# Kernel tuning notes

Measured on AMD Instinct MI355X. Metric: run time of the kernel, lower is better.

The kernel has to match this reference:

```python
import jax, jax.numpy as jnp
import numpy as np

B, D, H, E, K = 4096, 1024, 4096, 8, 2

def setup_inputs() -> dict:
    key = jax.random.key(0)
    ks = jax.random.split(key, 6)
    return {
        "x_modality": jax.random.normal(ks[0], (B, D), dtype=jnp.float32),
        "expert_indices": jax.random.randint(ks[1], (B, K), 0, E, dtype=jnp.int32),
        "hard_weights": jax.random.uniform(ks[2], (B, K), dtype=jnp.float32),
        "w1": jax.random.normal(ks[3], (E, D, H), dtype=jnp.float32) * (1.0 / np.sqrt(D)),
        "b1": jnp.zeros((E, H), dtype=jnp.float32),
        "w2": jax.random.normal(ks[4], (E, H, D), dtype=jnp.float32) * (1.0 / np.sqrt(H)),
        "b2": jnp.zeros((E, D), dtype=jnp.float32),
    }

def reference(x_modality, expert_indices, hard_weights, w1, b1, w2, b2):
    b = x_modality.shape[0]
    # Per-token gate per expert: sum of hard_weights over top_k slots routed to that expert.
    gates = jnp.zeros((b, E), dtype=x_modality.dtype)
    gates = gates.at[jnp.arange(b)[:, None], expert_indices].add(hard_weights)  # [b, E]
    # Dense expert compute (small fixed E), then gated combine.
    h = jax.nn.gelu(jnp.einsum("bd,edh->ebh", x_modality, w1) + b1[:, None, :], approximate=False)
    y = jnp.einsum("ebh,ehd->ebd", h, w2) + b2[:, None, :]  # [E, b, D]
    return jnp.einsum("be,ebd->bd", gates, y)
```

## Files before the change

kernel.cpp:

```cpp
#include <hip/hip_runtime.h>
#include <hip/hip_bf16.h>
#include <math.h>

#define NB 4096
#define ND 1024
#define NH 4096
#define NE 8
#define NKK 2
#define NROWS (NB*NKK)

typedef __attribute__((ext_vector_type(8))) short short8;
typedef __attribute__((ext_vector_type(4))) float f32x4;

__device__ __forceinline__ void gload_lds16(const void* g, void* l) {
    __builtin_amdgcn_global_load_lds(
        (const __attribute__((address_space(1))) unsigned int*)g,
        (__attribute__((address_space(3))) unsigned int*)l, 16, 0, 0);
}

__device__ __forceinline__ unsigned short f2bf(float f) {
    __hip_bfloat16 h = __float2bfloat16(f);
    return *reinterpret_cast<unsigned short*>(&h);
}


__global__ void k_cvt_x(const float* __restrict__ in, __hip_bfloat16* __restrict__ out, int n8) {
    int i = blockIdx.x * 256 + threadIdx.x;
    if (i >= n8) return;
    const float4* p = reinterpret_cast<const float4*>(in) + (size_t)i * 2;
    float4 a = p[0], b = p[1];
    ushort4 lo, hi;
    lo.x = f2bf(a.x); lo.y = f2bf(a.y); lo.z = f2bf(a.z); lo.w = f2bf(a.w);
    hi.x = f2bf(b.x); hi.y = f2bf(b.y); hi.z = f2bf(b.z); hi.w = f2bf(b.w);
    reinterpret_cast<ushort4*>(out)[(size_t)i*2]   = lo;
    reinterpret_cast<ushort4*>(out)[(size_t)i*2+1] = hi;
}

__global__ void k_transpose_cvt(const float* __restrict__ in, __hip_bfloat16* __restrict__ out,
                                int R, int C) {
    __shared__ float tile[64][65];
    const size_t ebase = (size_t)blockIdx.z * R * C;
    const int r0 = blockIdx.y * 64, c0 = blockIdx.x * 64;
    const int tx = threadIdx.x & 63, tg = threadIdx.x >> 6;
    #pragma unroll
    for (int i = 0; i < 16; ++i) {
        int r = tg + i * 4;
        tile[r][tx] = in[ebase + (size_t)(r0 + r) * C + (c0 + tx)];
    }
    __syncthreads();
    const int q = threadIdx.x & 15, cw = threadIdx.x >> 4;
    #pragma unroll
    for (int i = 0; i < 4; ++i) {
        int c = cw + i * 16;
        ushort4 v;
        v.x = f2bf(tile[q*4+0][c]);
        v.y = f2bf(tile[q*4+1][c]);
        v.z = f2bf(tile[q*4+2][c]);
        v.w = f2bf(tile[q*4+3][c]);
        *reinterpret_cast<ushort4*>(&out[ebase + (size_t)(c0 + c) * R + (r0 + q*4)]) = v;
    }
}


__global__ void k_route_count(const int* __restrict__ idx, int* cnt) {
    int b = blockIdx.x * 256 + threadIdx.x;
    if (b < NB) {
        atomicAdd(&cnt[idx[2*b]], 1);
        atomicAdd(&cnt[idx[2*b+1]], 1);
    }
}

__global__ void k_route_scan(const int* __restrict__ cnt, int* offs, int* cursor) {
    if (threadIdx.x == 0) {
        int s = 0;
        for (int e = 0; e < NE; ++e) { offs[e] = s; cursor[e] = s; s += cnt[e]; }
        offs[NE] = s;
    }
}

__global__ void k_route_fill(const int* __restrict__ idx, const float* __restrict__ hw,
                             int* cursor, int* tok, float* gw) {
    int b = blockIdx.x * 256 + threadIdx.x;
    if (b < NB) {
        #pragma unroll
        for (int k = 0; k < NKK; ++k) {
            int e = idx[2*b + k];
            int p = atomicAdd(&cursor[e], 1);
            tok[p] = b;
            gw[p]  = hw[2*b + k];
        }
    }
}


template<int STAGE>
__global__ __launch_bounds__(256, 2) void moe_gemm(
    const __hip_bfloat16* __restrict__ Asrc,
    const __hip_bfloat16* __restrict__ Bt,
    const float* __restrict__ bias,
    __hip_bfloat16* __restrict__ Hout,
    float* __restrict__ Out,
    const int* __restrict__ offs,
    const int* __restrict__ tok,
    const float* __restrict__ gw)
{
    constexpr int N = (STAGE == 1) ? NH : ND;
    constexpr int K = (STAGE == 1) ? ND : NH;

    const int e = blockIdx.z;
    const int end = offs[e + 1];
    const int rowbase = offs[e] + blockIdx.y * 128;
    if (rowbase >= end) return;
    const int nt = blockIdx.x;

    __shared__ __align__(16) __hip_bfloat16 sA[128 * 64];
    __shared__ __align__(16) __hip_bfloat16 sB[128 * 64];

    const int tid = threadIdx.x;
    const int w = tid >> 6;
    const int l = tid & 63;

    const int srow = tid >> 3;
    const int schunk = (tid & 7) ^ (srow & 7);
    const __hip_bfloat16* aptr[4];
    const __hip_bfloat16* bptr[4];
    #pragma unroll
    for (int i = 0; i < 4; ++i) {
        int r = srow + i * 32;
        int re = rowbase + r; if (re > end - 1) re = end - 1;
        if (STAGE == 1) aptr[i] = Asrc + (size_t)tok[re] * ND + schunk * 8;
        else            aptr[i] = Asrc + (size_t)re * NH + schunk * 8;
        bptr[i] = Bt + ((size_t)e * N + (nt * 128 + r)) * K + schunk * 8;
    }
    __hip_bfloat16 *adst[4], *bdst[4];
    #pragma unroll
    for (int i = 0; i < 4; ++i) {
        adst[i] = sA + (i * 256 + w * 64) * 8;
        bdst[i] = sB + (i * 256 + w * 64) * 8;
    }

    const int wm = (w >> 1) * 64;
    const int wn = (w & 1) * 64;
    const int l15 = l & 15, l4 = l >> 4;

    f32x4 acc[4][4];
    #pragma unroll
    for (int mi = 0; mi < 4; ++mi)
        #pragma unroll
        for (int ni = 0; ni < 4; ++ni) acc[mi][ni] = (f32x4){0.f, 0.f, 0.f, 0.f};

    int aoff[4][2], boff[4][2];
    #pragma unroll
    for (int mi = 0; mi < 4; ++mi) {
        int row = wm + mi * 16 + l15;
        #pragma unroll
        for (int ks = 0; ks < 2; ++ks)
            aoff[mi][ks] = row * 128 + (((ks * 4 + l4) ^ (row & 7)) * 16);
    }
    #pragma unroll
    for (int ni = 0; ni < 4; ++ni) {
        int row = wn + ni * 16 + l15;
        #pragma unroll
        for (int ks = 0; ks < 2; ++ks)
            boff[ni][ks] = row * 128 + (((ks * 4 + l4) ^ (row & 7)) * 16);
    }

    const char* sAb = (const char*)sA;
    const char* sBb = (const char*)sB;

    for (int kt = 0; kt < K / 64; ++kt) {
        #pragma unroll
        for (int i = 0; i < 4; ++i) {
            gload_lds16(aptr[i] + kt * 64, adst[i]);
            gload_lds16(bptr[i] + kt * 64, bdst[i]);
        }
        __syncthreads();
        short8 af[4][2], bfr[4][2];
        #pragma unroll
        for (int mi = 0; mi < 4; ++mi)
            #pragma unroll
            for (int ks = 0; ks < 2; ++ks)
                af[mi][ks] = *(const short8*)(sAb + aoff[mi][ks]);
        #pragma unroll
        for (int ni = 0; ni < 4; ++ni)
            #pragma unroll
            for (int ks = 0; ks < 2; ++ks)
                bfr[ni][ks] = *(const short8*)(sBb + boff[ni][ks]);
        #pragma unroll
        for (int mi = 0; mi < 4; ++mi)
            #pragma unroll
            for (int ni = 0; ni < 4; ++ni)
                #pragma unroll
                for (int ks = 0; ks < 2; ++ks)
                    acc[mi][ni] = __builtin_amdgcn_mfma_f32_16x16x32_bf16(
                        af[mi][ks], bfr[ni][ks], acc[mi][ni], 0, 0, 0);
        __syncthreads();
    }

    const int ncol0 = nt * 128 + wn;
    #pragma unroll
    for (int mi = 0; mi < 4; ++mi) {
        #pragma unroll
        for (int ni = 0; ni < 4; ++ni) {
            int gn = ncol0 + ni * 16 + l15;
            float bv = bias[e * N + gn];
            #pragma unroll
            for (int j = 0; j < 4; ++j) {
                int re = rowbase + wm + mi * 16 + l4 * 4 + j;
                if (re < end) {
                    float v = acc[mi][ni][j] + bv;
                    if (STAGE == 1) {
                        float g = 0.5f * v * (1.0f + erff(v * 0.70710678118654752f));
                        Hout[(size_t)re * NH + gn] = __float2bfloat16(g);
                    } else {
                        atomicAdd(&Out[(size_t)tok[re] * ND + gn], gw[re] * v);
                    }
                }
            }
        }
    }
}


extern "C" void kernel_launch(void* const* d_in, const int* in_sizes, int n_in,
                              void* d_out, int out_size, void* d_ws, size_t ws_size,
                              hipStream_t stream) {
    const float* x   = (const float*)d_in[0];
    const int*   idx = (const int*)d_in[1];
    const float* hw  = (const float*)d_in[2];
    const float* w1  = (const float*)d_in[3];
    const float* b1  = (const float*)d_in[4];
    const float* w2  = (const float*)d_in[5];
    const float* b2  = (const float*)d_in[6];
    float* out = (float*)d_out;

    char* ws = (char*)d_ws;
    size_t off = 0;
    __hip_bfloat16* xb  = (__hip_bfloat16*)(ws + off); off += (size_t)NB * ND * 2;
    __hip_bfloat16* w1t = (__hip_bfloat16*)(ws + off); off += (size_t)NE * ND * NH * 2;
    __hip_bfloat16* w2t = (__hip_bfloat16*)(ws + off); off += (size_t)NE * NH * ND * 2;
    __hip_bfloat16* h   = (__hip_bfloat16*)(ws + off); off += (size_t)NROWS * NH * 2;
    int*   tok    = (int*)(ws + off);   off += NROWS * 4;
    float* gwb    = (float*)(ws + off); off += NROWS * 4;
    int*   cnt    = (int*)(ws + off);   off += 16 * 4;
    int*   offs   = (int*)(ws + off);   off += 16 * 4;
    int*   cursor = (int*)(ws + off);   off += 16 * 4;
    (void)ws_size; (void)in_sizes; (void)n_in; (void)out_size;

    hipMemsetAsync(d_out, 0, (size_t)NB * ND * sizeof(float), stream);
    hipMemsetAsync(cnt, 0, 16 * 4, stream);

    k_cvt_x<<<dim3((NB * ND / 8 + 255) / 256), 256, 0, stream>>>(x, xb, NB * ND / 8);
    k_transpose_cvt<<<dim3(NH / 64, ND / 64, NE), 256, 0, stream>>>(w1, w1t, ND, NH);
    k_transpose_cvt<<<dim3(ND / 64, NH / 64, NE), 256, 0, stream>>>(w2, w2t, NH, ND);
    k_route_count<<<dim3((NB + 255) / 256), 256, 0, stream>>>(idx, cnt);
    k_route_scan<<<1, 64, 0, stream>>>(cnt, offs, cursor);
    k_route_fill<<<dim3((NB + 255) / 256), 256, 0, stream>>>(idx, hw, cursor, tok, gwb);

    moe_gemm<1><<<dim3(NH / 128, NROWS / 128, NE), 256, 0, stream>>>(
        xb, w1t, b1, h, nullptr, offs, tok, gwb);
    moe_gemm<2><<<dim3(ND / 128, NROWS / 128, NE), 256, 0, stream>>>(
        h, w2t, b2, nullptr, out, offs, tok, gwb);
}
```

Baseline: 443.2 us.

## Compact MoE GEMM grid via tile list, XCD-aware block remap, fast GELU

Routing now emits a compact list of (expert, row-start) tiles. Each GEMM launches a 1D grid over MAXT tiles times the N tiles, with blockIdx remapped so consecutive blocks spread across the 8 XCDs, instead of a 3D grid where most blocks exit early. The erf-based GELU is replaced with an Abramowitz-Stegun polynomial approximation that uses a hardware reciprocal and exp, and launch bounds are raised to 4 waves per SIMD, which may force register spills. The approximation adds small error, within bf16 tolerance, and MAXT=72 caps the tile count, which holds for any routing since 8192 rows produce at most 64+8 tiles.

```diff
diff --git a/kernel.cpp b/kernel.cpp
--- a/kernel.cpp
+++ b/kernel.cpp
@@ -8,6 +8,7 @@
 #define NE 8
 #define NKK 2
 #define NROWS (NB*NKK)
+#define MAXT 72
 
 typedef __attribute__((ext_vector_type(8))) short short8;
 typedef __attribute__((ext_vector_type(4))) float f32x4;
@@ -21,6 +22,18 @@
 __device__ __forceinline__ unsigned short f2bf(float f) {
     __hip_bfloat16 h = __float2bfloat16(f);
     return *reinterpret_cast<unsigned short*>(&h);
+}
+
+__device__ __forceinline__ float fast_gelu(float x) {
+    float xs  = x * 0.70710678118654752f;
+    float axs = fabsf(xs);
+    float t   = __builtin_amdgcn_rcpf(1.0f + 0.3275911f * axs);
+    float p   = t * (0.254829592f + t * (-0.284496736f + t * (1.421413741f +
+                t * (-1.453152027f + t * 1.061405429f))));
+    float e   = __expf(-xs * xs);
+    float erf_abs = 1.0f - p * e;
+    float erf = copysignf(erf_abs, x);
+    return 0.5f * x * (1.0f + erf);
 }
 
 
@@ -70,11 +83,19 @@
     }
 }
 
-__global__ void k_route_scan(const int* __restrict__ cnt, int* offs, int* cursor) {
+__global__ void k_route_scan(const int* __restrict__ cnt, int* offs, int* cursor,
+                             int* tile_e, int* tile_row, int* ntiles) {
     if (threadIdx.x == 0) {
-        int s = 0;
-        for (int e = 0; e < NE; ++e) { offs[e] = s; cursor[e] = s; s += cnt[e]; }
+        int s = 0, t = 0;
+        for (int e = 0; e < NE; ++e) {
+            offs[e] = s; cursor[e] = s;
+            for (int r = 0; r < cnt[e]; r += 128) {
+                tile_e[t] = e; tile_row[t] = s + r; ++t;
+            }
+            s += cnt[e];
+        }
         offs[NE] = s;
+        *ntiles = t;
     }
 }
 
@@ -94,7 +115,7 @@
 
 
 template<int STAGE>
-__global__ __launch_bounds__(256, 2) void moe_gemm(
+__global__ __launch_bounds__(256, 4) void moe_gemm(
     const __hip_bfloat16* __restrict__ Asrc,
     const __hip_bfloat16* __restrict__ Bt,
     const float* __restrict__ bias,
@@ -102,16 +123,26 @@
     float* __restrict__ Out,
     const int* __restrict__ offs,
     const int* __restrict__ tok,
-    const float* __restrict__ gw)
+    const float* __restrict__ gw,
+    const int* __restrict__ tile_e,
+    const int* __restrict__ tile_row,
+    const int* __restrict__ ntiles)
 {
     constexpr int N = (STAGE == 1) ? NH : ND;
     constexpr int K = (STAGE == 1) ? ND : NH;
-
-    const int e = blockIdx.z;
+    constexpr int NT_N = N / 128;
+    constexpr int TOTAL = NT_N * MAXT;
+    constexpr int CPX = TOTAL / 8;
+
+    const int bid = blockIdx.x;
+    const int wgid = (bid & 7) * CPX + (bid >> 3);
+    const int tile = wgid % MAXT;
+    const int nt   = wgid / MAXT;
+    if (tile >= *ntiles) return;
+
+    const int e = tile_e[tile];
+    const int rowbase = tile_row[tile];
     const int end = offs[e + 1];
-    const int rowbase = offs[e] + blockIdx.y * 128;
-    if (rowbase >= end) return;
-    const int nt = blockIdx.x;
 
     __shared__ __align__(16) __hip_bfloat16 sA[128 * 64];
     __shared__ __align__(16) __hip_bfloat16 sB[128 * 64];
@@ -210,8 +241,7 @@
                 if (re < end) {
                     float v = acc[mi][ni][j] + bv;
                     if (STAGE == 1) {
-                        float g = 0.5f * v * (1.0f + erff(v * 0.70710678118654752f));
-                        Hout[(size_t)re * NH + gn] = __float2bfloat16(g);
+                        Hout[(size_t)re * NH + gn] = __float2bfloat16(fast_gelu(v));
                     } else {
                         atomicAdd(&Out[(size_t)tok[re] * ND + gn], gw[re] * v);
                     }
@@ -240,11 +270,14 @@
     __hip_bfloat16* w1t = (__hip_bfloat16*)(ws + off); off += (size_t)NE * ND * NH * 2;
     __hip_bfloat16* w2t = (__hip_bfloat16*)(ws + off); off += (size_t)NE * NH * ND * 2;
     __hip_bfloat16* h   = (__hip_bfloat16*)(ws + off); off += (size_t)NROWS * NH * 2;
-    int*   tok    = (int*)(ws + off);   off += NROWS * 4;
-    float* gwb    = (float*)(ws + off); off += NROWS * 4;
-    int*   cnt    = (int*)(ws + off);   off += 16 * 4;
-    int*   offs   = (int*)(ws + off);   off += 16 * 4;
-    int*   cursor = (int*)(ws + off);   off += 16 * 4;
+    int*   tok     = (int*)(ws + off);   off += NROWS * 4;
+    float* gwb     = (float*)(ws + off); off += NROWS * 4;
+    int*   cnt     = (int*)(ws + off);   off += 16 * 4;
+    int*   offs    = (int*)(ws + off);   off += 16 * 4;
+    int*   cursor  = (int*)(ws + off);   off += 16 * 4;
+    int*   tile_e  = (int*)(ws + off);   off += MAXT * 4;
+    int*   tile_row= (int*)(ws + off);   off += MAXT * 4;
+    int*   ntiles  = (int*)(ws + off);   off += 16 * 4;
     (void)ws_size; (void)in_sizes; (void)n_in; (void)out_size;
 
     hipMemsetAsync(d_out, 0, (size_t)NB * ND * sizeof(float), stream);
@@ -254,11 +287,11 @@
     k_transpose_cvt<<<dim3(NH / 64, ND / 64, NE), 256, 0, stream>>>(w1, w1t, ND, NH);
     k_transpose_cvt<<<dim3(ND / 64, NH / 64, NE), 256, 0, stream>>>(w2, w2t, NH, ND);
     k_route_count<<<dim3((NB + 255) / 256), 256, 0, stream>>>(idx, cnt);
-    k_route_scan<<<1, 64, 0, stream>>>(cnt, offs, cursor);
+    k_route_scan<<<1, 64, 0, stream>>>(cnt, offs, cursor, tile_e, tile_row, ntiles);
     k_route_fill<<<dim3((NB + 255) / 256), 256, 0, stream>>>(idx, hw, cursor, tok, gwb);
 
-    moe_gemm<1><<<dim3(NH / 128, NROWS / 128, NE), 256, 0, stream>>>(
-        xb, w1t, b1, h, nullptr, offs, tok, gwb);
-    moe_gemm<2><<<dim3(ND / 128, NROWS / 128, NE), 256, 0, stream>>>(
-        h, w2t, b2, nullptr, out, offs, tok, gwb);
-}
+    moe_gemm<1><<<dim3((NH / 128) * MAXT), 256, 0, stream>>>(
+        xb, w1t, b1, h, nullptr, offs, tok, gwb, tile_e, tile_row, ntiles);
+    moe_gemm<2><<<dim3((ND / 128) * MAXT), 256, 0, stream>>>(
+        h, w2t, b2, nullptr, out, offs, tok, gwb, tile_e, tile_row, ntiles);
+}
```

Measured after the change: 416.7 us. 6.0% less time.
